# Performance work log

Measured on AMD Instinct MI355X. Metric: run time of the kernel, lower is better.

Reference implementation:

```python
import jax, jax.numpy as jnp
import numpy as np

N_NODES = 122880  # 4096 graphs * 30 nodes
N_EDGES = 983040


def gcn_conv(x, W, b, src, dst, n):
    """PyG GCNConv: symmetric-normalized aggregation with self-loops."""
    h = x @ W  # [n, out]
    loop = jnp.arange(n, dtype=src.dtype)
    s = jnp.concatenate([src, loop])
    d = jnp.concatenate([dst, loop])
    deg = jnp.zeros((n,), dtype=h.dtype).at[d].add(1.0)  # >=1 due to self loops
    dinv = jax.lax.rsqrt(deg)
    norm = dinv[s] * dinv[d]  # [E+n]
    out = jax.ops.segment_sum(h[s] * norm[:, None], d, num_segments=n)
    return out + b


def setup_inputs() -> dict:
    key = jax.random.key(0)
    ks = jax.random.split(key, 8)
    x = jax.random.normal(ks[0], (N_NODES, 64), dtype=jnp.float32)
    edge_index = jax.random.randint(ks[1], (2, N_EDGES), 0, N_NODES, dtype=jnp.int64)
    W1 = jax.random.normal(ks[2], (64, 128), dtype=jnp.float32) * (1.0 / np.sqrt(64))
    b1 = jnp.zeros((128,), dtype=jnp.float32)
    W2 = jax.random.normal(ks[3], (128, 64), dtype=jnp.float32) * (1.0 / np.sqrt(128))
    b2 = jnp.zeros((64,), dtype=jnp.float32)
    Wfc = jax.random.normal(ks[4], (1920, 1728), dtype=jnp.float32) * (1.0 / np.sqrt(1920))
    bfc = jnp.zeros((1728,), dtype=jnp.float32)
    return {"x": x, "edge_index": edge_index, "W1": W1, "b1": b1,
            "W2": W2, "b2": b2, "Wfc": Wfc, "bfc": bfc}


def reference(x, edge_index, W1, b1, W2, b2, Wfc, bfc):
    n = x.shape[0]
    src, dst = edge_index[0], edge_index[1]
    h = gcn_conv(x, W1, b1, src, dst, n)
    h = jax.nn.relu(h)  # dropout is identity in eval mode
    h = gcn_conv(h, W2, b2, src, dst, n)
    h = jax.nn.relu(h)
    h = h.reshape(-1, 64 * 30)  # [B, 1920], 30 nodes per graph
    return h @ Wfc + bfc  # [B, 1728]
```

## Files before the change

kernel.cpp:

```cpp
#include <hip/hip_runtime.h>
#include <hip/hip_bf16.h>

#define N_NODES 122880
#define N_EDGES 983040
#define NBKT 480
#define BCAP 2560
#define EPB 4096
#define NPAD 1792

typedef __hip_bfloat16 bf16;
typedef __attribute__((ext_vector_type(8))) short short8;
typedef __attribute__((ext_vector_type(4))) float floatx4;

__device__ __forceinline__ void gl_lds16(const void* g, void* l) {
    __builtin_amdgcn_global_load_lds(
        (const __attribute__((address_space(1))) void*)g,
        (__attribute__((address_space(3))) void*)l, 16, 0, 0);
}

__device__ __forceinline__ float bflo(unsigned u) {
    return __uint_as_float(u << 16);
}
__device__ __forceinline__ float bfhi(unsigned u) {
    return __uint_as_float(u & 0xffff0000u);
}

__global__ __launch_bounds__(256) void k_psort(const int* __restrict__ ei,
                                               int* __restrict__ gcur,
                                               unsigned* __restrict__ gbuf) {
    __shared__ int cur[NBKT];
    __shared__ int gb[NBKT];
    const int t = threadIdx.x;
    for (int i = t; i < NBKT; i += 256) cur[i] = 0;
    __syncthreads();
    const int base = blockIdx.x * EPB;
    unsigned pay[16];
    short bk[16], pib[16];
#pragma unroll
    for (int j = 0; j < 16; ++j) {
        int e = base + j * 256 + t;
        int d = ei[N_EDGES + e];
        int s = ei[e];
        bk[j] = (short)(d >> 8);
        pay[j] = (unsigned)(d & 255) | ((unsigned)s << 8);
        pib[j] = (short)atomicAdd(&cur[d >> 8], 1);
    }
    __syncthreads();
    for (int i = t; i < NBKT; i += 256) {
        int c = cur[i];
        gb[i] = c ? atomicAdd(&gcur[i * 16], c) : 0;
    }
    __syncthreads();
#pragma unroll
    for (int j = 0; j < 16; ++j) {
        int pos = gb[bk[j]] + pib[j];
        if (pos < BCAP) gbuf[bk[j] * BCAP + pos] = pay[j];
    }
}

__global__ __launch_bounds__(256) void k_bcsr(const int* __restrict__ gcur,
                                              const unsigned* __restrict__ gbuf,
                                              int* __restrict__ adj,
                                              unsigned* __restrict__ co,
                                              float* __restrict__ dinv) {
    __shared__ int hist[256];
    __shared__ int arr[256];
    __shared__ int exc[256];
    const int b = blockIdx.x, t = threadIdx.x;
    hist[t] = 0;
    __syncthreads();
    int E = gcur[b * 16];
    if (E > BCAP) E = BCAP;
    int dl[10], sv[10];
    short pb[10];
    int n = 0;
    for (int idx = t; idx < E; idx += 256) {
        unsigned p = gbuf[b * BCAP + idx];
        dl[n] = p & 255;
        sv[n] = (int)(p >> 8);
        pb[n] = (short)atomicAdd(&hist[dl[n]], 1);
        ++n;
    }
    __syncthreads();
    const int cnt_t = hist[t];
    arr[t] = cnt_t;
    __syncthreads();
    for (int d = 1; d < 256; d <<= 1) {
        int v = (t >= d) ? arr[t - d] : 0;
        __syncthreads();
        arr[t] += v;
        __syncthreads();
    }
    const int ex = arr[t] - cnt_t;
    exc[t] = ex;
    const int node = b * 256 + t;
    co[node] = ((unsigned)ex << 16) | (unsigned)cnt_t;
    dinv[node] = rsqrtf((float)cnt_t + 1.0f);
    __syncthreads();
    for (int j = 0; j < n; ++j)
        adj[b * BCAP + exc[dl[j]] + pb[j]] = sv[j];
}

__global__ __launch_bounds__(256) void k_xtobf(const float* __restrict__ x,
                                               const float* __restrict__ dinv,
                                               bf16* __restrict__ xb) {
    int t = blockIdx.x * 256 + threadIdx.x;
    const float di = dinv[t >> 4];
    const float4 v = ((const float4*)x)[t];
    bf16* o = xb + t * 4;
    o[0] = __float2bfloat16(di * v.x);
    o[1] = __float2bfloat16(di * v.y);
    o[2] = __float2bfloat16(di * v.z);
    o[3] = __float2bfloat16(di * v.w);
}

__global__ __launch_bounds__(256) void k_convw(const float* __restrict__ W1,
                                               const float* __restrict__ W2,
                                               bf16* __restrict__ W1T,
                                               bf16* __restrict__ W2T) {
    int t = blockIdx.x * 256 + threadIdx.x;
    if (t < 64 * 128) {
        int k = t >> 7, n = t & 127;
        W1T[n * 64 + k] = __float2bfloat16(W1[t]);
    } else {
        int u = t - 64 * 128;
        int k = u >> 6, n = u & 63;
        W2T[n * 128 + k] = __float2bfloat16(W2[u]);
    }
}

__global__ __launch_bounds__(256) void k_transWfc(const float* __restrict__ W,
                                                  bf16* __restrict__ WT) {
    __shared__ float t[32][33];
    int tx = threadIdx.x, ty = threadIdx.y;
    int n0 = blockIdx.x * 32, k0 = blockIdx.y * 32;
    const bool nok = (n0 + tx) < 1728;
#pragma unroll
    for (int j = 0; j < 4; ++j)
        t[ty + j * 8][tx] =
            nok ? W[(long)(k0 + ty + j * 8) * 1728 + n0 + tx] : 0.0f;
    __syncthreads();
#pragma unroll
    for (int j = 0; j < 4; ++j)
        WT[(long)(n0 + ty + j * 8) * 1920 + k0 + tx] =
            __float2bfloat16(t[tx][ty + j * 8]);
}

template <bool BIAS_RELU>
__global__ __launch_bounds__(256) void k_agg(const bf16* __restrict__ xb,
                                             const float* __restrict__ dinv,
                                             const unsigned* __restrict__ co,
                                             const int* __restrict__ adj,
                                             const float* __restrict__ bias,
                                             bf16* __restrict__ out) {
    const int wave = threadIdx.x >> 6, lane = threadIdx.x & 63;
    const int sub = lane >> 4, l16 = lane & 15;
    const int node = blockIdx.x * 16 + wave * 4 + sub;

    const float di = dinv[node];
    const unsigned c_ = co[node];
    int c = (int)(c_ & 0xffffu);
    if (c > 32) c = 32;
    const int* al = adj + (node >> 8) * BCAP + (c_ >> 16);
    int sl  = (l16 < c)      ? al[l16]      : 0;
    int sl2 = (16 + l16 < c) ? al[16 + l16] : 0;

    const uint2 us = *(const uint2*)(xb + ((long)node << 6) + (l16 << 2));
    float a0 = bflo(us.x), a1 = bfhi(us.x);
    float a2 = bflo(us.y), a3 = bfhi(us.y);

    for (int p0 = 0; p0 < c; p0 += 8) {
        uint2 uu[8];
#pragma unroll
        for (int j = 0; j < 8; ++j) {
            int p = p0 + j;
            bool ok = p < c;
            int sv = (p < 16) ? sl : sl2;
            int s = __shfl(sv, p & 15, 16);
            uint2 u = *(const uint2*)(xb + ((long)s << 6) + (l16 << 2));
            uu[j].x = ok ? u.x : 0u;
            uu[j].y = ok ? u.y : 0u;
        }
#pragma unroll
        for (int j = 0; j < 8; ++j) {
            a0 += bflo(uu[j].x);
            a1 += bfhi(uu[j].x);
            a2 += bflo(uu[j].y);
            a3 += bfhi(uu[j].y);
        }
    }

    float r0 = di * a0, r1 = di * a1, r2 = di * a2, r3 = di * a3;
    if (BIAS_RELU) {
        r0 = fmaxf(r0 + bias[l16 * 4 + 0], 0.0f);
        r1 = fmaxf(r1 + bias[l16 * 4 + 1], 0.0f);
        r2 = fmaxf(r2 + bias[l16 * 4 + 2], 0.0f);
        r3 = fmaxf(r3 + bias[l16 * 4 + 3], 0.0f);
    }
    bf16* o = out + ((long)node << 6) + (l16 << 2);
    o[0] = __float2bfloat16(r0);
    o[1] = __float2bfloat16(r1);
    o[2] = __float2bfloat16(r2);
    o[3] = __float2bfloat16(r3);
}

__global__ __launch_bounds__(256) void k_mlp(const bf16* __restrict__ xa,
                                             const bf16* __restrict__ W1T,
                                             const bf16* __restrict__ W2T,
                                             const float* __restrict__ b1,
                                             const float* __restrict__ dinv,
                                             bf16* __restrict__ g) {
    __shared__ __align__(16) bf16 As[128 * 64];
    __shared__ __align__(16) bf16 C1s[128 * 136];
    const int tid = threadIdx.x;
    const int wave = tid >> 6, lane = tid & 63;
    const int quad = lane >> 4, l16 = lane & 15;
    const int bm = blockIdx.x * 128;
    const int wm = (wave & 1) * 64;
    const int wn1 = (wave >> 1) * 64;
    const int wn2 = (wave >> 1) * 32;

#pragma unroll
    for (int q = 0; q < 4; ++q) {
        int G = q * 256 + tid;
        int gc = (G & ~7) | ((G & 7) ^ ((G >> 3) & 7));
        gl_lds16(xa + (long)bm * 64 + gc * 8, As + ((q * 4 + wave) * 64) * 8);
    }
    short8 w1f[2][4];
#pragma unroll
    for (int kc = 0; kc < 2; ++kc)
#pragma unroll
        for (int in = 0; in < 4; ++in)
            w1f[kc][in] = *(const short8*)(W1T + (wn1 + in * 16 + l16) * 64 +
                                           kc * 32 + quad * 8);
    floatx4 acc1[4][4];
#pragma unroll
    for (int i = 0; i < 4; ++i)
#pragma unroll
        for (int j = 0; j < 4; ++j) acc1[i][j] = (floatx4){0.f, 0.f, 0.f, 0.f};
    __syncthreads();

#pragma unroll
    for (int kc = 0; kc < 2; ++kc)
#pragma unroll
        for (int im = 0; im < 4; ++im) {
            const int R = wm + im * 16 + l16;
            short8 af = *(const short8*)(As + R * 64 +
                                         (((kc * 4 + quad) ^ (R & 7)) * 8));
#pragma unroll
            for (int in = 0; in < 4; ++in)
                acc1[im][in] = __builtin_amdgcn_mfma_f32_16x16x32_bf16(
                    af, w1f[kc][in], acc1[im][in], 0, 0, 0);
        }

#pragma unroll
    for (int in = 0; in < 4; ++in) {
        const int col = wn1 + in * 16 + l16;
        const float bv = b1[col];
#pragma unroll
        for (int im = 0; im < 4; ++im) {
            const int row = wm + im * 16 + quad * 4;
#pragma unroll
            for (int r = 0; r < 4; ++r)
                C1s[(row + r) * 136 + col] =
                    __float2bfloat16(fmaxf(acc1[im][in][r] + bv, 0.0f));
        }
    }
    short8 w2f[4][2];
#pragma unroll
    for (int kc = 0; kc < 4; ++kc)
#pragma unroll
        for (int in = 0; in < 2; ++in)
            w2f[kc][in] = *(const short8*)(W2T + (wn2 + in * 16 + l16) * 128 +
                                           kc * 32 + quad * 8);
    floatx4 acc2[4][2];
#pragma unroll
    for (int i = 0; i < 4; ++i)
#pragma unroll
        for (int j = 0; j < 2; ++j) acc2[i][j] = (floatx4){0.f, 0.f, 0.f, 0.f};
    __syncthreads();

#pragma unroll
    for (int kc = 0; kc < 4; ++kc)
#pragma unroll
        for (int im = 0; im < 4; ++im) {
            short8 af = *(const short8*)(C1s + (wm + im * 16 + l16) * 136 +
                                         kc * 32 + quad * 8);
#pragma unroll
            for (int in = 0; in < 2; ++in)
                acc2[im][in] = __builtin_amdgcn_mfma_f32_16x16x32_bf16(
                    af, w2f[kc][in], acc2[im][in], 0, 0, 0);
        }

    float dv[4][4];
#pragma unroll
    for (int im = 0; im < 4; ++im)
#pragma unroll
        for (int r = 0; r < 4; ++r)
            dv[im][r] = dinv[bm + wm + im * 16 + quad * 4 + r];

#pragma unroll
    for (int in = 0; in < 2; ++in) {
        const int col = wn2 + in * 16 + l16;
#pragma unroll
        for (int im = 0; im < 4; ++im) {
            const int row = bm + wm + im * 16 + quad * 4;
#pragma unroll
            for (int r = 0; r < 4; ++r)
                g[(long)(row + r) * 64 + col] =
                    __float2bfloat16(dv[im][r] * acc2[im][in][r]);
        }
    }
}

template <bool RELU, bool BIAS, typename OutT>
__global__ __launch_bounds__(512) void gemm_bt(const bf16* __restrict__ A,
                                               const bf16* __restrict__ BT,
                                               const float* __restrict__ bias,
                                               OutT* __restrict__ C,
                                               int M, int N, int K) {
    __shared__ __align__(16) bf16 As[2][128 * 32];
    __shared__ __align__(16) bf16 Bs[2][128 * 32];
    const int tid = threadIdx.x;
    const int wave = tid >> 6, lane = tid & 63;
    const int quad = lane >> 4, l16 = lane & 15;
    const int bid = blockIdx.x;
    const int bx = (bid & 7) * 4 + ((bid >> 3) & 3);
    const int by = bid >> 5;
    const int bm = bx * 128, bn = by * 128;
    const int wm = (wave & 1) * 64, wn = (wave >> 1) * 32;

    floatx4 acc[4][2];
#pragma unroll
    for (int i = 0; i < 4; ++i)
#pragma unroll
        for (int j = 0; j < 2; ++j) acc[i][j] = (floatx4){0.f, 0.f, 0.f, 0.f};

    const int r4 = tid >> 2;
    const int cc = tid & 3;
    const int slot = r4 * 32 + ((cc ^ ((r4 >> 1) & 3)) * 8);

    const bf16* gA = A + (long)(bm + r4) * K + cc * 8;
    const bf16* gB = BT + (long)(bn + r4) * K + cc * 8;

    const int rsw = (l16 >> 1) & 3;
    const int NT = K >> 5;

    uint4 ra = *(const uint4*)gA;
    uint4 rb = *(const uint4*)gB;
    *(uint4*)(As[0] + slot) = ra;
    *(uint4*)(Bs[0] + slot) = rb;
    ra = *(const uint4*)(gA + 32);
    rb = *(const uint4*)(gB + 32);
    __syncthreads();

    for (int t = 0; t < NT; t += 2) {
        {
            short8 af[4], bfr[2];
#pragma unroll
            for (int im = 0; im < 4; ++im)
                af[im] = *(const short8*)(As[0] + (wm + im * 16 + l16) * 32 +
                                          (quad ^ rsw) * 8);
#pragma unroll
            for (int in = 0; in < 2; ++in)
                bfr[in] = *(const short8*)(Bs[0] + (wn + in * 16 + l16) * 32 +
                                           (quad ^ rsw) * 8);
            *(uint4*)(As[1] + slot) = ra;
            *(uint4*)(Bs[1] + slot) = rb;
            if (t + 2 < NT) {
                ra = *(const uint4*)(gA + (t + 2) * 32);
                rb = *(const uint4*)(gB + (t + 2) * 32);
            }
#pragma unroll
            for (int im = 0; im < 4; ++im)
#pragma unroll
                for (int in = 0; in < 2; ++in)
                    acc[im][in] = __builtin_amdgcn_mfma_f32_16x16x32_bf16(
                        af[im], bfr[in], acc[im][in], 0, 0, 0);
            __syncthreads();
        }
        {
            short8 af[4], bfr[2];
#pragma unroll
            for (int im = 0; im < 4; ++im)
                af[im] = *(const short8*)(As[1] + (wm + im * 16 + l16) * 32 +
                                          (quad ^ rsw) * 8);
#pragma unroll
            for (int in = 0; in < 2; ++in)
                bfr[in] = *(const short8*)(Bs[1] + (wn + in * 16 + l16) * 32 +
                                           (quad ^ rsw) * 8);
            if (t + 2 < NT) {
                *(uint4*)(As[0] + slot) = ra;
                *(uint4*)(Bs[0] + slot) = rb;
            }
            if (t + 3 < NT) {
                ra = *(const uint4*)(gA + (t + 3) * 32);
                rb = *(const uint4*)(gB + (t + 3) * 32);
            }
#pragma unroll
            for (int im = 0; im < 4; ++im)
#pragma unroll
                for (int in = 0; in < 2; ++in)
                    acc[im][in] = __builtin_amdgcn_mfma_f32_16x16x32_bf16(
                        af[im], bfr[in], acc[im][in], 0, 0, 0);
            __syncthreads();
        }
    }

#pragma unroll
    for (int in = 0; in < 2; ++in) {
        int gcol = bn + wn + in * 16 + l16;
        bool wok = gcol < N;
        float bv = (BIAS && wok) ? bias[gcol] : 0.0f;
#pragma unroll
        for (int im = 0; im < 4; ++im) {
            int mrow = bm + wm + im * 16 + quad * 4;
#pragma unroll
            for (int r = 0; r < 4; ++r) {
                float v = acc[im][in][r] + bv;
                if (RELU) v = fmaxf(v, 0.0f);
                if (wok) {
                    if constexpr (sizeof(OutT) == 2)
                        C[(long)(mrow + r) * N + gcol] = __float2bfloat16(v);
                    else
                        C[(long)(mrow + r) * N + gcol] = v;
                }
            }
        }
    }
}

extern "C" void kernel_launch(void* const* d_in, const int* in_sizes, int n_in,
                              void* d_out, int out_size, void* d_ws, size_t ws_size,
                              hipStream_t stream) {
    const float* x   = (const float*)d_in[0];
    const int*   ei  = (const int*)d_in[1];
    const float* W1  = (const float*)d_in[2];
    const float* b1  = (const float*)d_in[3];
    const float* W2  = (const float*)d_in[4];
    const float* b2  = (const float*)d_in[5];
    const float* Wfc = (const float*)d_in[6];
    const float* bfc = (const float*)d_in[7];

    char* p = (char*)d_ws;
    int*      gcur = (int*)p;      p += (size_t)NBKT * 16 * 4;
    unsigned* gbuf = (unsigned*)p; p += (size_t)NBKT * BCAP * 4;
    int*      adj  = (int*)p;      p += (size_t)NBKT * BCAP * 4;
    unsigned* co   = (unsigned*)p; p += (size_t)N_NODES * 4;
    float*    dinv = (float*)p;    p += (size_t)N_NODES * 4;
    bf16*     xb   = (bf16*)p;     p += (size_t)N_NODES * 64 * 2;
    bf16*     xa   = (bf16*)p;     p += (size_t)N_NODES * 64 * 2;
    bf16*     g    = (bf16*)p;     p += (size_t)N_NODES * 64 * 2;
    bf16*     h2   = (bf16*)p;     p += (size_t)N_NODES * 64 * 2;
    bf16*     W1T  = (bf16*)p;     p += 128 * 64 * 2;
    bf16*     W2T  = (bf16*)p;     p += 64 * 128 * 2;
    bf16*     WfcT = (bf16*)p;     p += (size_t)NPAD * 1920 * 2;

    hipMemsetAsync(gcur, 0, (size_t)NBKT * 16 * 4, stream);
    k_psort<<<N_EDGES / EPB, 256, 0, stream>>>(ei, gcur, gbuf);
    k_bcsr<<<NBKT, 256, 0, stream>>>(gcur, gbuf, adj, co, dinv);
    k_xtobf<<<N_NODES * 64 / 4 / 256, 256, 0, stream>>>(x, dinv, xb);
    k_convw<<<64, 256, 0, stream>>>(W1, W2, W1T, W2T);
    k_transWfc<<<dim3(56, 60), dim3(32, 8), 0, stream>>>(Wfc, WfcT);

    k_agg<false><<<N_NODES / 16, 256, 0, stream>>>(xb, dinv, co, adj, nullptr, xa);
    k_mlp<<<N_NODES / 128, 256, 0, stream>>>(xa, W1T, W2T, b1, dinv, g);
    k_agg<true><<<N_NODES / 16, 256, 0, stream>>>(g, dinv, co, adj, b2, h2);
    gemm_bt<false, true, float><<<448, 512, 0, stream>>>(
        h2, WfcT, bfc, (float*)d_out, 4096, 1728, 1920);
}
```

Before: 232.2 us.

## Merge preprocessing kernels into fewer launches to cut launch gaps

Merges the edge bucket-sort, the W1/W2 conversion and the Wfc transpose into one launch, with the work split by block index. The x-to-bf16 scaling moves into the CSR build kernel, which reads dinv from shared memory. This removes three kernel launches and their serialization gaps, and lets the independent weight prep overlap with the sort. In exchange, the CSR kernel now also streams x with a serial 16-iteration loop per block.

```diff
diff --git a/kernel.cpp b/kernel.cpp
--- a/kernel.cpp
+++ b/kernel.cpp
@@ -25,36 +25,68 @@
     return __uint_as_float(u & 0xffff0000u);
 }
 
-__global__ __launch_bounds__(256) void k_psort(const int* __restrict__ ei,
-                                               int* __restrict__ gcur,
-                                               unsigned* __restrict__ gbuf) {
-    __shared__ int cur[NBKT];
-    __shared__ int gb[NBKT];
-    const int t = threadIdx.x;
-    for (int i = t; i < NBKT; i += 256) cur[i] = 0;
-    __syncthreads();
-    const int base = blockIdx.x * EPB;
-    unsigned pay[16];
-    short bk[16], pib[16];
-#pragma unroll
-    for (int j = 0; j < 16; ++j) {
-        int e = base + j * 256 + t;
-        int d = ei[N_EDGES + e];
-        int s = ei[e];
-        bk[j] = (short)(d >> 8);
-        pay[j] = (unsigned)(d & 255) | ((unsigned)s << 8);
-        pib[j] = (short)atomicAdd(&cur[d >> 8], 1);
-    }
-    __syncthreads();
-    for (int i = t; i < NBKT; i += 256) {
-        int c = cur[i];
-        gb[i] = c ? atomicAdd(&gcur[i * 16], c) : 0;
-    }
-    __syncthreads();
-#pragma unroll
-    for (int j = 0; j < 16; ++j) {
-        int pos = gb[bk[j]] + pib[j];
-        if (pos < BCAP) gbuf[bk[j] * BCAP + pos] = pay[j];
+__global__ __launch_bounds__(256) void k_psort_prep(
+        const int* __restrict__ ei, int* __restrict__ gcur,
+        unsigned* __restrict__ gbuf,
+        const float* __restrict__ W1, const float* __restrict__ W2,
+        const float* __restrict__ Wfc,
+        bf16* __restrict__ W1T, bf16* __restrict__ W2T,
+        bf16* __restrict__ WfcT) {
+    __shared__ __align__(16) char smem[4352];
+    const int b = blockIdx.x, t = threadIdx.x;
+    if (b < 240) {
+        int* cur = (int*)smem;
+        int* gb  = (int*)(smem + 1920);
+        for (int i = t; i < NBKT; i += 256) cur[i] = 0;
+        __syncthreads();
+        const int base = b * EPB;
+        unsigned pay[16];
+        short bk[16], pib[16];
+#pragma unroll
+        for (int j = 0; j < 16; ++j) {
+            int e = base + j * 256 + t;
+            int d = ei[N_EDGES + e];
+            int s = ei[e];
+            bk[j] = (short)(d >> 8);
+            pay[j] = (unsigned)(d & 255) | ((unsigned)s << 8);
+            pib[j] = (short)atomicAdd(&cur[d >> 8], 1);
+        }
+        __syncthreads();
+        for (int i = t; i < NBKT; i += 256) {
+            int c = cur[i];
+            gb[i] = c ? atomicAdd(&gcur[i * 16], c) : 0;
+        }
+        __syncthreads();
+#pragma unroll
+        for (int j = 0; j < 16; ++j) {
+            int pos = gb[bk[j]] + pib[j];
+            if (pos < BCAP) gbuf[bk[j] * BCAP + pos] = pay[j];
+        }
+    } else if (b < 304) {
+        int u = (b - 240) * 256 + t;
+        if (u < 64 * 128) {
+            int k = u >> 7, n = u & 127;
+            W1T[n * 64 + k] = __float2bfloat16(W1[u]);
+        } else {
+            int v = u - 64 * 128;
+            int k = v >> 6, n = v & 63;
+            W2T[n * 128 + k] = __float2bfloat16(W2[v]);
+        }
+    } else {
+        float (*ts)[33] = (float(*)[33])smem;
+        const int bid2 = b - 304;
+        const int n0 = (bid2 % 56) * 32, k0 = (bid2 / 56) * 32;
+        const int tx = t & 31, ty = t >> 5;
+        const bool nok = (n0 + tx) < 1728;
+#pragma unroll
+        for (int j = 0; j < 4; ++j)
+            ts[ty + j * 8][tx] =
+                nok ? Wfc[(long)(k0 + ty + j * 8) * 1728 + n0 + tx] : 0.0f;
+        __syncthreads();
+#pragma unroll
+        for (int j = 0; j < 4; ++j)
+            WfcT[(long)(n0 + ty + j * 8) * 1920 + k0 + tx] =
+                __float2bfloat16(ts[tx][ty + j * 8]);
     }
 }
 
@@ -62,10 +94,13 @@
                                               const unsigned* __restrict__ gbuf,
                                               int* __restrict__ adj,
                                               unsigned* __restrict__ co,
-                                              float* __restrict__ dinv) {
+                                              float* __restrict__ dinv,
+                                              const float* __restrict__ x,
+                                              bf16* __restrict__ xb) {
     __shared__ int hist[256];
     __shared__ int arr[256];
     __shared__ int exc[256];
+    __shared__ float dinvs[256];
     const int b = blockIdx.x, t = threadIdx.x;
     hist[t] = 0;
     __syncthreads();
@@ -95,55 +130,25 @@
     exc[t] = ex;
     const int node = b * 256 + t;
     co[node] = ((unsigned)ex << 16) | (unsigned)cnt_t;
-    dinv[node] = rsqrtf((float)cnt_t + 1.0f);
+    const float di = rsqrtf((float)cnt_t + 1.0f);
+    dinv[node] = di;
+    dinvs[t] = di;
     __syncthreads();
     for (int j = 0; j < n; ++j)
         adj[b * BCAP + exc[dl[j]] + pb[j]] = sv[j];
-}
-
-__global__ __launch_bounds__(256) void k_xtobf(const float* __restrict__ x,
-                                               const float* __restrict__ dinv,
-                                               bf16* __restrict__ xb) {
-    int t = blockIdx.x * 256 + threadIdx.x;
-    const float di = dinv[t >> 4];
-    const float4 v = ((const float4*)x)[t];
-    bf16* o = xb + t * 4;
-    o[0] = __float2bfloat16(di * v.x);
-    o[1] = __float2bfloat16(di * v.y);
-    o[2] = __float2bfloat16(di * v.z);
-    o[3] = __float2bfloat16(di * v.w);
-}
-
-__global__ __launch_bounds__(256) void k_convw(const float* __restrict__ W1,
-                                               const float* __restrict__ W2,
-                                               bf16* __restrict__ W1T,
-                                               bf16* __restrict__ W2T) {
-    int t = blockIdx.x * 256 + threadIdx.x;
-    if (t < 64 * 128) {
-        int k = t >> 7, n = t & 127;
-        W1T[n * 64 + k] = __float2bfloat16(W1[t]);
-    } else {
-        int u = t - 64 * 128;
-        int k = u >> 6, n = u & 63;
-        W2T[n * 128 + k] = __float2bfloat16(W2[u]);
-    }
-}
-
-__global__ __launch_bounds__(256) void k_transWfc(const float* __restrict__ W,
-                                                  bf16* __restrict__ WT) {
-    __shared__ float t[32][33];
-    int tx = threadIdx.x, ty = threadIdx.y;
-    int n0 = blockIdx.x * 32, k0 = blockIdx.y * 32;
-    const bool nok = (n0 + tx) < 1728;
-#pragma unroll
-    for (int j = 0; j < 4; ++j)
-        t[ty + j * 8][tx] =
-            nok ? W[(long)(k0 + ty + j * 8) * 1728 + n0 + tx] : 0.0f;
-    __syncthreads();
-#pragma unroll
-    for (int j = 0; j < 4; ++j)
-        WT[(long)(n0 + ty + j * 8) * 1920 + k0 + tx] =
-            __float2bfloat16(t[tx][ty + j * 8]);
+
+    const long xbase = (long)b * 256 * 64;
+    for (int r = 0; r < 16; ++r) {
+        int u = r * 256 + t;
+        int nl = u >> 4;
+        const float4 v = ((const float4*)(x + xbase))[u];
+        const float d2 = dinvs[nl];
+        bf16* o = xb + xbase + u * 4;
+        o[0] = __float2bfloat16(d2 * v.x);
+        o[1] = __float2bfloat16(d2 * v.y);
+        o[2] = __float2bfloat16(d2 * v.z);
+        o[3] = __float2bfloat16(d2 * v.w);
+    }
 }
 
 template <bool BIAS_RELU>
@@ -457,11 +462,9 @@
     bf16*     WfcT = (bf16*)p;     p += (size_t)NPAD * 1920 * 2;
 
     hipMemsetAsync(gcur, 0, (size_t)NBKT * 16 * 4, stream);
-    k_psort<<<N_EDGES / EPB, 256, 0, stream>>>(ei, gcur, gbuf);
-    k_bcsr<<<NBKT, 256, 0, stream>>>(gcur, gbuf, adj, co, dinv);
-    k_xtobf<<<N_NODES * 64 / 4 / 256, 256, 0, stream>>>(x, dinv, xb);
-    k_convw<<<64, 256, 0, stream>>>(W1, W2, W1T, W2T);
-    k_transWfc<<<dim3(56, 60), dim3(32, 8), 0, stream>>>(Wfc, WfcT);
+    k_psort_prep<<<3664, 256, 0, stream>>>(ei, gcur, gbuf, W1, W2, Wfc,
+                                           W1T, W2T, WfcT);
+    k_bcsr<<<NBKT, 256, 0, stream>>>(gcur, gbuf, adj, co, dinv, x, xb);
 
     k_agg<false><<<N_NODES / 16, 256, 0, stream>>>(xb, dinv, co, adj, nullptr, xa);
     k_mlp<<<N_NODES / 128, 256, 0, stream>>>(xa, W1T, W2T, b1, dinv, g);
```

Result: faster. 225.6 us (-2.8%).
